# Kernel optimization log

Hardware: AMD Instinct MI355X
Metric: run time of the kernel (lower is better)

## Reference

```python
import jax, jax.numpy as jnp
import numpy as np

TEMPERATURE = 0.5
EPS = 1e-8  # matches torch CosineSimilarity eps


def setup_inputs() -> dict:
    key = jax.random.key(0)
    k1, k2 = jax.random.split(key)
    N, D = 4096, 256
    z1 = jax.random.normal(k1, (N, D), dtype=jnp.float32)
    z2 = jax.random.normal(k2, (N, D), dtype=jnp.float32)
    return {"z1": z1, "z2": z2}


def reference(z1, z2):
    N = z1.shape[0]
    z = jnp.concatenate([z1, z2], axis=0)            # [2N, D]
    norm = jnp.linalg.norm(z, axis=-1, keepdims=True)
    zn = z / jnp.maximum(norm, EPS)                  # L2-normalized
    sim = (zn @ zn.T) / TEMPERATURE                  # [2N, 2N] cosine sim / temp
    # mask self-similarity on the diagonal
    diag = jnp.eye(2 * N, dtype=bool)
    sim = jnp.where(diag, -jnp.inf, sim)
    # positive pair labels: row i pairs with i+N (first half) or i-N (second half)
    labels = jnp.concatenate([jnp.arange(N) + N, jnp.arange(N)])
    logp = jax.nn.log_softmax(sim, axis=-1)
    loss = -jnp.mean(logp[jnp.arange(2 * N), labels])
    return loss
```

## Files before the change

### kernel.cpp

```cpp
#include <hip/hip_runtime.h>
#include <hip/hip_bf16.h>


#define NROWS 8192
#define NHALF 4096
#define DDIM  256
#define GT    128
#define NTILES (NROWS / GT)
#define NBLK  (NTILES * (NTILES + 1) / 2)
#define BN    64
#define LDSB  528

typedef __bf16 bf16;
typedef __bf16 bf16x4 __attribute__((ext_vector_type(4)));
typedef __bf16 bf16x8 __attribute__((ext_vector_type(8)));
typedef float  f32x4  __attribute__((ext_vector_type(4)));

__constant__ const float kC   = 2.8853900817779268f;
__constant__ const float kLn2 = 0.6931471805599453f;

__global__ void k_normalize(const float* __restrict__ z1, const float* __restrict__ z2,
                            bf16* __restrict__ znA, bf16* __restrict__ znB,
                            float* __restrict__ rowsum, float* __restrict__ out) {
  const int wave = threadIdx.x >> 6, lane = threadIdx.x & 63;
  const int row = blockIdx.x * 4 + wave;
  const float* src = (row < NHALF) ? z1 + (size_t)row * DDIM
                                   : z2 + (size_t)(row - NHALF) * DDIM;
  f32x4 v = *(const f32x4*)(src + lane * 4);
  float ss = v.x * v.x + v.y * v.y + v.z * v.z + v.w * v.w;
#pragma unroll
  for (int off = 1; off < 64; off <<= 1) ss += __shfl_xor(ss, off);
  const float inv  = 1.0f / fmaxf(sqrtf(ss), 1e-8f);
  const float invc = inv * kC;
  bf16x4 oa, ob;
  oa.x = (bf16)(v.x * invc); oa.y = (bf16)(v.y * invc);
  oa.z = (bf16)(v.z * invc); oa.w = (bf16)(v.w * invc);
  ob.x = (bf16)(v.x * inv);  ob.y = (bf16)(v.y * inv);
  ob.z = (bf16)(v.z * inv);  ob.w = (bf16)(v.w * inv);
  *(bf16x4*)(znA + (size_t)row * DDIM + lane * 4) = oa;
  *(bf16x4*)(znB + (size_t)row * DDIM + lane * 4) = ob;
  if (lane == 0) rowsum[row] = 0.0f;
  if (blockIdx.x == 0 && threadIdx.x == 0) out[0] = 0.0f;
}

__global__ __launch_bounds__(256, 2) void k_gram(const bf16* __restrict__ znA,
                                                 const bf16* __restrict__ znB,
                                                 float* __restrict__ rowsum) {
  __shared__ __align__(16) unsigned char lds[2][BN * LDSB];
  __shared__ float colsum[GT];
  const int tid  = threadIdx.x;
  const int wave = tid >> 6, lane = tid & 63;
  const int quad = lane >> 4, l15 = lane & 15;

  int p = blockIdx.x, I = 0;
  while (p >= NTILES - I) { p -= NTILES - I; ++I; }
  const int J = I + p;
  const bool diag = (I == J);
  const int c0 = J * GT;

  if (tid < GT) colsum[tid] = 0.0f;

  bf16x8 a[2][8];
#pragma unroll
  for (int s = 0; s < 2; ++s) {
    const int row = I * GT + wave * 32 + s * 16 + l15;
    const bf16x8* ap = (const bf16x8*)(znA + (size_t)row * DDIM);
#pragma unroll
    for (int k = 0; k < 8; ++k) a[s][k] = ap[k * 4 + quad];
  }

  const int tr = tid >> 2, tc = tid & 3;
  uint4 g[8];
  {
    const unsigned char* gp = (const unsigned char*)(znB + (size_t)(c0 + tr) * DDIM);
#pragma unroll
    for (int j = 0; j < 8; ++j) g[j] = *(const uint4*)(gp + (tc + 4 * j) * 16);
  }
#pragma unroll
  for (int j = 0; j < 8; ++j)
    *(uint4*)(&lds[0][tr * LDSB + (tc + 4 * j) * 16]) = g[j];

  float sum[2][4] = {{0.f, 0.f, 0.f, 0.f}, {0.f, 0.f, 0.f, 0.f}};
  const f32x4 zero4 = {0.f, 0.f, 0.f, 0.f};

#pragma unroll
  for (int it = 0; it < 2; ++it) {
    __syncthreads();
    if (it == 0) {
      const unsigned char* gp = (const unsigned char*)(znB + (size_t)(c0 + BN + tr) * DDIM);
#pragma unroll
      for (int j = 0; j < 8; ++j) g[j] = *(const uint4*)(gp + (tc + 4 * j) * 16);
    }

    f32x4 acc[2][4];
#pragma unroll
    for (int s = 0; s < 2; ++s)
#pragma unroll
      for (int cs = 0; cs < 4; ++cs) acc[s][cs] = zero4;

#pragma unroll
    for (int k = 0; k < 8; ++k) {
      bf16x8 b[4];
#pragma unroll
      for (int cs = 0; cs < 4; ++cs)
        b[cs] = *(const bf16x8*)(&lds[it][(cs * 16 + l15) * LDSB + k * 64 + quad * 16]);
#pragma unroll
      for (int s = 0; s < 2; ++s)
#pragma unroll
        for (int cs = 0; cs < 4; ++cs)
          acc[s][cs] = __builtin_amdgcn_mfma_f32_16x16x32_bf16(a[s][k], b[cs], acc[s][cs], 0, 0, 0);
    }

    if (it == 0) {
#pragma unroll
      for (int j = 0; j < 8; ++j)
        *(uint4*)(&lds[1][tr * LDSB + (tc + 4 * j) * 16]) = g[j];
    }

#pragma unroll
    for (int cs = 0; cs < 4; ++cs) {
      float cp = 0.0f;
#pragma unroll
      for (int s = 0; s < 2; ++s)
#pragma unroll
        for (int r = 0; r < 4; ++r) {
          const float v = __builtin_amdgcn_exp2f(acc[s][cs][r]);
          sum[s][r] += v;
          cp += v;
        }
      if (!diag) {
        cp += __shfl_xor(cp, 16);
        cp += __shfl_xor(cp, 32);
        if (lane < 16) atomicAdd(&colsum[it * BN + cs * 16 + l15], cp);
      }
    }
  }

#pragma unroll
  for (int s = 0; s < 2; ++s)
#pragma unroll
    for (int r = 0; r < 4; ++r) {
      float v = sum[s][r];
      v += __shfl_xor(v, 1); v += __shfl_xor(v, 2);
      v += __shfl_xor(v, 4); v += __shfl_xor(v, 8);
      if (l15 == 0)
        atomicAdd(&rowsum[I * GT + wave * 32 + s * 16 + quad * 4 + r], v);
    }

  __syncthreads();
  if (!diag && tid < GT) atomicAdd(&rowsum[c0 + tid], colsum[tid]);
}

__device__ __forceinline__ float dot4(bf16x4 a, bf16x4 b) {
  return (float)a.x * (float)b.x + (float)a.y * (float)b.y +
         (float)a.z * (float)b.z + (float)a.w * (float)b.w;
}

__global__ void k_finalize(const bf16* __restrict__ znA, const bf16* __restrict__ znB,
                           const float* __restrict__ rowsum, float* __restrict__ out) {
  const int wave = threadIdx.x >> 6, lane = threadIdx.x & 63;
  const int gw = blockIdx.x * 4 + wave;
  float acc = 0.0f;
  for (int t = 0; t < 16; ++t) {
    const int q = gw * 16 + t, pq = q + NHALF;
    bf16x4 aq = *(const bf16x4*)(znA + (size_t)q  * DDIM + lane * 4);
    bf16x4 bq = *(const bf16x4*)(znB + (size_t)q  * DDIM + lane * 4);
    bf16x4 ap = *(const bf16x4*)(znA + (size_t)pq * DDIM + lane * 4);
    bf16x4 bp = *(const bf16x4*)(znB + (size_t)pq * DDIM + lane * 4);
    float dqq = dot4(aq, bq);
    float dpp = dot4(ap, bp);
    float dqp = dot4(aq, bp);
#pragma unroll
    for (int off = 1; off < 64; off <<= 1) {
      dqq += __shfl_xor(dqq, off);
      dpp += __shfl_xor(dpp, off);
      dqp += __shfl_xor(dqp, off);
    }
    if (lane == 0) {
      const float lseq = __builtin_amdgcn_logf(rowsum[q]  - __builtin_amdgcn_exp2f(dqq)) * kLn2;
      const float lsep = __builtin_amdgcn_logf(rowsum[pq] - __builtin_amdgcn_exp2f(dpp)) * kLn2;
      acc += lseq + lsep - 2.0f * dqp * kLn2;
    }
  }
  __shared__ float ws4[4];
  if (lane == 0) ws4[wave] = acc;
  __syncthreads();
  if (threadIdx.x == 0)
    atomicAdd(out, (ws4[0] + ws4[1] + ws4[2] + ws4[3]) * (1.0f / (float)NROWS));
}

extern "C" void kernel_launch(void* const* d_in, const int* in_sizes, int n_in,
                              void* d_out, int out_size, void* d_ws, size_t ws_size,
                              hipStream_t stream) {
  const float* z1 = (const float*)d_in[0];
  const float* z2 = (const float*)d_in[1];
  unsigned char* ws = (unsigned char*)d_ws;

  bf16* znA = (bf16*)ws;
  bf16* znB = (bf16*)(ws + (size_t)NROWS * DDIM * sizeof(bf16));
  float* rowsum = (float*)(ws + 2 * (size_t)NROWS * DDIM * sizeof(bf16));
  float* out = (float*)d_out;

  hipLaunchKernelGGL(k_normalize, dim3(NROWS / 4), dim3(256), 0, stream, z1, z2, znA, znB, rowsum, out);
  hipLaunchKernelGGL(k_gram, dim3(NBLK), dim3(256), 0, stream, znA, znB, rowsum);
  hipLaunchKernelGGL(k_finalize, dim3(64), dim3(256), 0, stream, znA, znB, rowsum, out);
}
```

Before: 128.3 us.

## Restructure Gram kernel into persistent strip work-split with direct-to-LDS async loads

Replaces the per-tile 128x128 triangular grid with 512 persistent blocks, each walking 4-5 consecutive 256x64 tiles along upper-triangular row strips. The 256-row A fragment stays in registers across tiles, and B tiles are double-buffered through global_load_lds straight into LDS in MFMA fragment order. The two normalized copies are merged into one scaled by sqrt(C), which halves the normalized-data footprint. The change aims to cut launch and tail imbalance, redundant A reloads and VGPR staging, at the cost of more registers (a[4][8], acc[4][4]) and more complex indexing.

```diff
diff --git a/kernel.cpp b/kernel.cpp
--- a/kernel.cpp
+++ b/kernel.cpp
@@ -5,23 +5,27 @@
 #define NROWS 8192
 #define NHALF 4096
 #define DDIM  256
-#define GT    128
-#define NTILES (NROWS / GT)
-#define NBLK  (NTILES * (NTILES + 1) / 2)
-#define BN    64
-#define LDSB  528
+#define NSTRIP 32
+#define TILE  256
+#define TOTIT 2112
 
 typedef __bf16 bf16;
 typedef __bf16 bf16x4 __attribute__((ext_vector_type(4)));
 typedef __bf16 bf16x8 __attribute__((ext_vector_type(8)));
 typedef float  f32x4  __attribute__((ext_vector_type(4)));
 
-__constant__ const float kC   = 2.8853900817779268f;
-__constant__ const float kLn2 = 0.6931471805599453f;
+__constant__ const float kSqrtC = 1.69864359f;
+__constant__ const float kLn2   = 0.6931471805599453f;
+
+__device__ __forceinline__ void load_lds16(const bf16* g, bf16* l) {
+  __builtin_amdgcn_global_load_lds(
+      (const __attribute__((address_space(1))) unsigned int*)g,
+      (__attribute__((address_space(3))) unsigned int*)l, 16, 0, 0);
+}
 
 __global__ void k_normalize(const float* __restrict__ z1, const float* __restrict__ z2,
-                            bf16* __restrict__ znA, bf16* __restrict__ znB,
-                            float* __restrict__ rowsum, float* __restrict__ out) {
+                            bf16* __restrict__ zn, float* __restrict__ rowsum,
+                            float* __restrict__ out) {
   const int wave = threadIdx.x >> 6, lane = threadIdx.x & 63;
   const int row = blockIdx.x * 4 + wave;
   const float* src = (row < NHALF) ? z1 + (size_t)row * DDIM
@@ -30,125 +34,138 @@
   float ss = v.x * v.x + v.y * v.y + v.z * v.z + v.w * v.w;
 #pragma unroll
   for (int off = 1; off < 64; off <<= 1) ss += __shfl_xor(ss, off);
-  const float inv  = 1.0f / fmaxf(sqrtf(ss), 1e-8f);
-  const float invc = inv * kC;
-  bf16x4 oa, ob;
-  oa.x = (bf16)(v.x * invc); oa.y = (bf16)(v.y * invc);
-  oa.z = (bf16)(v.z * invc); oa.w = (bf16)(v.w * invc);
-  ob.x = (bf16)(v.x * inv);  ob.y = (bf16)(v.y * inv);
-  ob.z = (bf16)(v.z * inv);  ob.w = (bf16)(v.w * inv);
-  *(bf16x4*)(znA + (size_t)row * DDIM + lane * 4) = oa;
-  *(bf16x4*)(znB + (size_t)row * DDIM + lane * 4) = ob;
+  const float inv = kSqrtC / fmaxf(sqrtf(ss), 1e-8f);
+  bf16x4 o;
+  o.x = (bf16)(v.x * inv); o.y = (bf16)(v.y * inv);
+  o.z = (bf16)(v.z * inv); o.w = (bf16)(v.w * inv);
+  *(bf16x4*)(zn + (size_t)row * DDIM + lane * 4) = o;
   if (lane == 0) rowsum[row] = 0.0f;
   if (blockIdx.x == 0 && threadIdx.x == 0) out[0] = 0.0f;
 }
 
-__global__ __launch_bounds__(256, 2) void k_gram(const bf16* __restrict__ znA,
-                                                 const bf16* __restrict__ znB,
+__global__ __launch_bounds__(256, 2) void k_gram(const bf16* __restrict__ zn,
                                                  float* __restrict__ rowsum) {
-  __shared__ __align__(16) unsigned char lds[2][BN * LDSB];
-  __shared__ float colsum[GT];
+  __shared__ __align__(16) bf16 bstage[2][32 * 512];
+  __shared__ float colsum[320];
   const int tid  = threadIdx.x;
   const int wave = tid >> 6, lane = tid & 63;
   const int quad = lane >> 4, l15 = lane & 15;
 
-  int p = blockIdx.x, I = 0;
-  while (p >= NTILES - I) { p -= NTILES - I; ++I; }
-  const int J = I + p;
-  const bool diag = (I == J);
-  const int c0 = J * GT;
-
-  if (tid < GT) colsum[tid] = 0.0f;
-
-  bf16x8 a[2][8];
-#pragma unroll
-  for (int s = 0; s < 2; ++s) {
-    const int row = I * GT + wave * 32 + s * 16 + l15;
-    const bf16x8* ap = (const bf16x8*)(znA + (size_t)row * DDIM);
-#pragma unroll
-    for (int k = 0; k < 8; ++k) a[s][k] = ap[k * 4 + quad];
-  }
-
-  const int tr = tid >> 2, tc = tid & 3;
-  uint4 g[8];
-  {
-    const unsigned char* gp = (const unsigned char*)(znB + (size_t)(c0 + tr) * DDIM);
-#pragma unroll
-    for (int j = 0; j < 8; ++j) g[j] = *(const uint4*)(gp + (tc + 4 * j) * 16);
-  }
-#pragma unroll
-  for (int j = 0; j < 8; ++j)
-    *(uint4*)(&lds[0][tr * LDSB + (tc + 4 * j) * 16]) = g[j];
-
-  float sum[2][4] = {{0.f, 0.f, 0.f, 0.f}, {0.f, 0.f, 0.f, 0.f}};
+  int t0, cnt;
+  if (blockIdx.x < 64) { t0 = blockIdx.x * 5; cnt = 5; }
+  else                 { t0 = 320 + ((int)blockIdx.x - 64) * 4; cnt = 4; }
+
+  int R = 0, rem = t0;
+  while (rem >= 4 * (NSTRIP - R)) { rem -= 4 * (NSTRIP - R); ++R; }
+  int cloc = rem;
+
+  for (int i = tid; i < 320; i += 256) colsum[i] = 0.0f;
+
+  bf16x8 a[4][8];
+  auto loadA = [&](int Rv) {
+#pragma unroll
+    for (int s = 0; s < 4; ++s) {
+      const int row = Rv * TILE + wave * 64 + s * 16 + l15;
+      const bf16x8* ap = (const bf16x8*)(zn + (size_t)row * DDIM);
+#pragma unroll
+      for (int k = 0; k < 8; ++k) a[s][k] = ap[k * 4 + quad];
+    }
+  };
+  loadA(R);
+
+  float sum[4][4];
+#pragma unroll
+  for (int s = 0; s < 4; ++s)
+#pragma unroll
+    for (int r = 0; r < 4; ++r) sum[s][r] = 0.0f;
+
+  auto flush_rows = [&]() {
+#pragma unroll
+    for (int s = 0; s < 4; ++s)
+#pragma unroll
+      for (int r = 0; r < 4; ++r) {
+        float v = sum[s][r];
+        v += __shfl_xor(v, 1); v += __shfl_xor(v, 2);
+        v += __shfl_xor(v, 4); v += __shfl_xor(v, 8);
+        if (l15 == 0)
+          atomicAdd(&rowsum[R * TILE + wave * 64 + s * 16 + quad * 4 + r], v);
+        sum[s][r] = 0.0f;
+      }
+  };
+
+  auto stage = [&](int buf, int colbase) {
+#pragma unroll
+    for (int c = 0; c < 8; ++c) {
+      const int chunk = wave * 8 + c;
+      const int kk = chunk >> 2, cs = chunk & 3;
+      const bf16* g = zn + (size_t)(colbase + cs * 16 + l15) * DDIM + kk * 32 + quad * 8;
+      load_lds16(g, &bstage[buf][chunk * 512]);
+    }
+  };
+  stage(0, R * TILE + cloc * 64);
+
   const f32x4 zero4 = {0.f, 0.f, 0.f, 0.f};
 
-#pragma unroll
-  for (int it = 0; it < 2; ++it) {
+  for (int tl = 0; tl < cnt; ++tl) {
     __syncthreads();
-    if (it == 0) {
-      const unsigned char* gp = (const unsigned char*)(znB + (size_t)(c0 + BN + tr) * DDIM);
-#pragma unroll
-      for (int j = 0; j < 8; ++j) g[j] = *(const uint4*)(gp + (tc + 4 * j) * 16);
-    }
-
-    f32x4 acc[2][4];
-#pragma unroll
-    for (int s = 0; s < 2; ++s)
-#pragma unroll
-      for (int cs = 0; cs < 4; ++cs) acc[s][cs] = zero4;
-
+    const int cur = tl & 1;
+    if (tl + 1 < cnt) {
+      int Rn = R, cn = cloc + 1;
+      if (cn == 4 * (NSTRIP - Rn)) { cn = 0; ++Rn; }
+      stage(cur ^ 1, Rn * TILE + cn * 64);
+    }
+    const bool dt = (cloc < 4);
+
+    f32x4 acc[4][4];
 #pragma unroll
     for (int k = 0; k < 8; ++k) {
       bf16x8 b[4];
 #pragma unroll
       for (int cs = 0; cs < 4; ++cs)
-        b[cs] = *(const bf16x8*)(&lds[it][(cs * 16 + l15) * LDSB + k * 64 + quad * 16]);
-#pragma unroll
-      for (int s = 0; s < 2; ++s)
+        b[cs] = *(const bf16x8*)(&bstage[cur][(k * 4 + cs) * 512 + lane * 8]);
+#pragma unroll
+      for (int s = 0; s < 4; ++s)
 #pragma unroll
         for (int cs = 0; cs < 4; ++cs)
-          acc[s][cs] = __builtin_amdgcn_mfma_f32_16x16x32_bf16(a[s][k], b[cs], acc[s][cs], 0, 0, 0);
-    }
-
-    if (it == 0) {
-#pragma unroll
-      for (int j = 0; j < 8; ++j)
-        *(uint4*)(&lds[1][tr * LDSB + (tc + 4 * j) * 16]) = g[j];
+          acc[s][cs] = __builtin_amdgcn_mfma_f32_16x16x32_bf16(
+              a[s][k], b[cs], k ? acc[s][cs] : zero4, 0, 0, 0);
     }
 
 #pragma unroll
     for (int cs = 0; cs < 4; ++cs) {
       float cp = 0.0f;
 #pragma unroll
-      for (int s = 0; s < 2; ++s)
+      for (int s = 0; s < 4; ++s)
 #pragma unroll
         for (int r = 0; r < 4; ++r) {
           const float v = __builtin_amdgcn_exp2f(acc[s][cs][r]);
           sum[s][r] += v;
           cp += v;
         }
-      if (!diag) {
+      if (!dt) {
         cp += __shfl_xor(cp, 16);
         cp += __shfl_xor(cp, 32);
-        if (lane < 16) atomicAdd(&colsum[it * BN + cs * 16 + l15], cp);
+        if (lane < 16) atomicAdd(&colsum[tl * 64 + cs * 16 + l15], cp);
       }
     }
+
+    ++cloc;
+    if (cloc == 4 * (NSTRIP - R) && tl + 1 < cnt) {
+      flush_rows();
+      ++R; cloc = 0;
+      loadA(R);
+    }
   }
-
-#pragma unroll
-  for (int s = 0; s < 2; ++s)
-#pragma unroll
-    for (int r = 0; r < 4; ++r) {
-      float v = sum[s][r];
-      v += __shfl_xor(v, 1); v += __shfl_xor(v, 2);
-      v += __shfl_xor(v, 4); v += __shfl_xor(v, 8);
-      if (l15 == 0)
-        atomicAdd(&rowsum[I * GT + wave * 32 + s * 16 + quad * 4 + r], v);
-    }
+  flush_rows();
 
   __syncthreads();
-  if (!diag && tid < GT) atomicAdd(&rowsum[c0 + tid], colsum[tid]);
+  for (int idx = tid; idx < cnt * 64; idx += 256) {
+    const int tloc = idx >> 6;
+    int Rv = 0, r2 = t0 + tloc;
+    while (r2 >= 4 * (NSTRIP - Rv)) { r2 -= 4 * (NSTRIP - Rv); ++Rv; }
+    const int col = Rv * TILE + r2 * 64 + (idx & 63);
+    atomicAdd(&rowsum[col], colsum[idx]);
+  }
 }
 
 __device__ __forceinline__ float dot4(bf16x4 a, bf16x4 b) {
@@ -156,20 +173,18 @@
          (float)a.z * (float)b.z + (float)a.w * (float)b.w;
 }
 
-__global__ void k_finalize(const bf16* __restrict__ znA, const bf16* __restrict__ znB,
-                           const float* __restrict__ rowsum, float* __restrict__ out) {
+__global__ void k_finalize(const bf16* __restrict__ zn, const float* __restrict__ rowsum,
+                           float* __restrict__ out) {
   const int wave = threadIdx.x >> 6, lane = threadIdx.x & 63;
   const int gw = blockIdx.x * 4 + wave;
   float acc = 0.0f;
   for (int t = 0; t < 16; ++t) {
     const int q = gw * 16 + t, pq = q + NHALF;
-    bf16x4 aq = *(const bf16x4*)(znA + (size_t)q  * DDIM + lane * 4);
-    bf16x4 bq = *(const bf16x4*)(znB + (size_t)q  * DDIM + lane * 4);
-    bf16x4 ap = *(const bf16x4*)(znA + (size_t)pq * DDIM + lane * 4);
-    bf16x4 bp = *(const bf16x4*)(znB + (size_t)pq * DDIM + lane * 4);
-    float dqq = dot4(aq, bq);
-    float dpp = dot4(ap, bp);
-    float dqp = dot4(aq, bp);
+    bf16x4 zq = *(const bf16x4*)(zn + (size_t)q  * DDIM + lane * 4);
+    bf16x4 zp = *(const bf16x4*)(zn + (size_t)pq * DDIM + lane * 4);
+    float dqq = dot4(zq, zq);
+    float dpp = dot4(zp, zp);
+    float dqp = dot4(zq, zp);
 #pragma unroll
     for (int off = 1; off < 64; off <<= 1) {
       dqq += __shfl_xor(dqq, off);
@@ -196,12 +211,11 @@
   const float* z2 = (const float*)d_in[1];
   unsigned char* ws = (unsigned char*)d_ws;
 
-  bf16* znA = (bf16*)ws;
-  bf16* znB = (bf16*)(ws + (size_t)NROWS * DDIM * sizeof(bf16));
-  float* rowsum = (float*)(ws + 2 * (size_t)NROWS * DDIM * sizeof(bf16));
+  bf16* zn = (bf16*)ws;
+  float* rowsum = (float*)(ws + (size_t)NROWS * DDIM * sizeof(bf16));
   float* out = (float*)d_out;
 
-  hipLaunchKernelGGL(k_normalize, dim3(NROWS / 4), dim3(256), 0, stream, z1, z2, znA, znB, rowsum, out);
-  hipLaunchKernelGGL(k_gram, dim3(NBLK), dim3(256), 0, stream, znA, znB, rowsum);
-  hipLaunchKernelGGL(k_finalize, dim3(64), dim3(256), 0, stream, znA, znB, rowsum, out);
-}
+  hipLaunchKernelGGL(k_normalize, dim3(NROWS / 4), dim3(256), 0, stream, z1, z2, zn, rowsum, out);
+  hipLaunchKernelGGL(k_gram, dim3(512), dim3(256), 0, stream, zn, rowsum);
+  hipLaunchKernelGGL(k_finalize, dim3(64), dim3(256), 0, stream, zn, rowsum, out);
+}
```

Result: faster. 117.0 us (-8.8%).
